# Performance work log

Hardware: AMD Instinct MI355X
Metric: run time of the kernel (lower is better)

The kernel has to match this reference:

```python
import jax, jax.numpy as jnp
import numpy as np
from jax import lax


def _conv(x, w, b):
    # x: [N,C,H,W], w: [O,I,kh,kw], valid conv, stride 1
    y = lax.conv_general_dilated(x, w, (1, 1), 'VALID',
                                 dimension_numbers=('NCHW', 'OIHW', 'NCHW'))
    return y + b[None, :, None, None]


def _maxpool2(x):
    return lax.reduce_window(x, -jnp.inf, lax.max, (1, 1, 2, 2), (1, 1, 2, 2), 'VALID')


def _affine_grid(theta, H, W):
    # torch F.affine_grid, align_corners=False: pixel-center normalized coords
    dt = theta.dtype
    xs = (2.0 * jnp.arange(W, dtype=dt) + 1.0) / W - 1.0  # [W]
    ys = (2.0 * jnp.arange(H, dtype=dt) + 1.0) / H - 1.0  # [H]
    gx = (theta[:, 0, 0][:, None, None] * xs[None, None, :]
          + theta[:, 0, 1][:, None, None] * ys[None, :, None]
          + theta[:, 0, 2][:, None, None])  # [N,H,W]
    gy = (theta[:, 1, 0][:, None, None] * xs[None, None, :]
          + theta[:, 1, 1][:, None, None] * ys[None, :, None]
          + theta[:, 1, 2][:, None, None])  # [N,H,W]
    return gx, gy


def _grid_sample(img, gx, gy):
    # torch F.grid_sample, bilinear, zeros padding, align_corners=False
    N, C, H, W = img.shape
    ix = ((gx + 1.0) * W - 1.0) * 0.5
    iy = ((gy + 1.0) * H - 1.0) * 0.5
    x0 = jnp.floor(ix)
    y0 = jnp.floor(iy)
    x1 = x0 + 1.0
    y1 = y0 + 1.0
    wx1 = ix - x0
    wx0 = 1.0 - wx1
    wy1 = iy - y0
    wy0 = 1.0 - wy1
    flat = img.reshape(N, C, H * W)

    def tap(xf, yf):
        xi = xf.astype(jnp.int32)
        yi = yf.astype(jnp.int32)
        inb = (xi >= 0) & (xi < W) & (yi >= 0) & (yi < H)
        idx = jnp.clip(yi, 0, H - 1) * W + jnp.clip(xi, 0, W - 1)  # [N,H,W]
        v = jnp.take_along_axis(flat, idx.reshape(N, 1, H * W), axis=2)
        return v.reshape(N, C, H, W) * inb.astype(img.dtype)[:, None]

    out = (tap(x0, y0) * (wx0 * wy0)[:, None]
           + tap(x1, y0) * (wx1 * wy0)[:, None]
           + tap(x0, y1) * (wx0 * wy1)[:, None]
           + tap(x1, y1) * (wx1 * wy1)[:, None])
    return out


def setup_inputs() -> dict:
    key = jax.random.key(0)
    ks = jax.random.split(key, 8)
    b, n, d, c = 64, 256, 28, 3
    x = jax.random.normal(ks[0], (b, n, d, d, c), dtype=jnp.float32)
    conv1_w = jax.random.normal(ks[1], (8, 3, 7, 7), dtype=jnp.float32) * 0.08
    conv1_b = jnp.zeros((8,), dtype=jnp.float32)
    conv2_w = jax.random.normal(ks[2], (10, 8, 5, 5), dtype=jnp.float32) * 0.07
    conv2_b = jnp.zeros((10,), dtype=jnp.float32)
    fc1_w = jax.random.normal(ks[3], (32, 90), dtype=jnp.float32) * 0.1
    fc1_b = jnp.zeros((32,), dtype=jnp.float32)
    # fc2 initialized near identity transform (as in the torch module),
    # with a small perturbation so theta depends on the input
    fc2_w = jax.random.normal(ks[4], (6, 32), dtype=jnp.float32) * 0.01
    fc2_b = jnp.array([1.0, 0.0, 0.0, 0.0, 1.0, 0.0], dtype=jnp.float32)
    return {"x": x, "conv1_w": conv1_w, "conv1_b": conv1_b,
            "conv2_w": conv2_w, "conv2_b": conv2_b,
            "fc1_w": fc1_w, "fc1_b": fc1_b,
            "fc2_w": fc2_w, "fc2_b": fc2_b}


def reference(x, conv1_w, conv1_b, conv2_w, conv2_b, fc1_w, fc1_b, fc2_w, fc2_b):
    b, n, d, _, c = x.shape
    xi = x.reshape(-1, d, d, c).transpose(0, 3, 1, 2)  # [b*n, 3, 28, 28]
    # localization net: conv -> maxpool -> relu, twice
    h = jax.nn.relu(_maxpool2(_conv(xi, conv1_w, conv1_b)))   # [N,8,11,11]
    h = jax.nn.relu(_maxpool2(_conv(h, conv2_w, conv2_b)))    # [N,10,3,3]
    h = h.reshape(-1, 10 * 3 * 3)
    h = jax.nn.relu(h @ fc1_w.T + fc1_b)
    theta = (h @ fc2_w.T + fc2_b).reshape(-1, 2, 3)
    gx, gy = _affine_grid(theta, d, d)
    out = _grid_sample(xi, gx, gy)                            # [N,3,28,28]
    return out.transpose(0, 2, 3, 1).reshape(b, n, d, d, c)
```

## Files before the change

### kernel.cpp

```cpp
#include <hip/hip_runtime.h>


typedef _Float16 half2_t __attribute__((ext_vector_type(2)));

static __device__ inline half2_t h2(uint32_t u) {
    union { uint32_t u; half2_t h; } cv; cv.u = u; return cv.h;
}
static __device__ inline uint32_t packh2(float a, float b) {
    union { half2_t h; uint32_t u; } cv;
    cv.h = (half2_t){(_Float16)a, (_Float16)b};
    return cv.u;
}

#if __has_builtin(__builtin_amdgcn_fdot2)
#define FDOT2(a, b, c) __builtin_amdgcn_fdot2((a), (b), (c), false)
#else
#define FDOT2(a, b, c) ((float)(a)[0] * (float)(b)[0] + (float)(a)[1] * (float)(b)[1] + (c))
#endif

#if __has_builtin(__builtin_amdgcn_alignbit)
#define ALIGN16(hi, lo) __builtin_amdgcn_alignbit((hi), (lo), 16)
#else
#define ALIGN16(hi, lo) (((lo) >> 16) | ((hi) << 16))
#endif

__launch_bounds__(256)
__global__ void stn_pack_kernel(
    const float* __restrict__ w2, const float* __restrict__ fc1w,
    uint32_t* __restrict__ w2p, uint32_t* __restrict__ fc1p)
{
    const int t = threadIdx.x;
    for (int k = t; k < 1000; k += 256) {
        const int o = k / 100;
        const int rem = k - 100 * o;
        const int c2kh = rem / 5;
        const int kw = rem - 5 * c2kh;
        const int c2 = c2kh / 5;
        const int kh = c2kh - 5 * c2;
        w2p[k] = packh2(w2[((o * 8 + 2 * c2) * 5 + kh) * 5 + kw],
                        w2[((o * 8 + 2 * c2 + 1) * 5 + kh) * 5 + kw]);
    }
    for (int k = t; k < 1472; k += 256) {
        const int of = k / 46;
        const int p = k - 46 * of;
        uint32_t v = 0;
        if (p < 45) v = packh2(fc1w[of * 90 + 2 * p], fc1w[of * 90 + 2 * p + 1]);
        fc1p[k] = v;
    }
}

__launch_bounds__(256, 4)
__global__ void stn_loc_kernel(
    const float* __restrict__ x,
    const float* __restrict__ w1, const float* __restrict__ b1,
    const uint32_t* __restrict__ w2p, const float* __restrict__ b2,
    const uint32_t* __restrict__ fc1p, const float* __restrict__ fc1b,
    const float* __restrict__ fc2w, const float* __restrict__ fc2b,
    float* __restrict__ theta_ws)
{
    __shared__ __align__(16) _Float16 s_imgh[4][3 * 28 * 40];
    __shared__ __align__(16) uint32_t s_w1p[8 * 21 * 4];
    __shared__ __align__(16) uint32_t s_h1p[4 * 4 * 10 * 12];
    __shared__ __align__(16) uint32_t s_h2p[4][48];
    __shared__ float s_fch[4][32];

    const int t = threadIdx.x;
    const int nb = blockIdx.x;

    for (int im = 0; im < 4; ++im) {
        const float* img = x + ((size_t)(nb * 4 + im)) * 2352;
        for (int p = t; p < 784; p += 256) {
            const int h = p / 28, w = p - 28 * h;
            s_imgh[im][(0 * 28 + h) * 40 + w] = (_Float16)img[3 * p + 0];
            s_imgh[im][(1 * 28 + h) * 40 + w] = (_Float16)img[3 * p + 1];
            s_imgh[im][(2 * 28 + h) * 40 + w] = (_Float16)img[3 * p + 2];
        }
        for (int idx = t; idx < 504; idx += 256) {
            const int cc = idx / 168;
            const int rem = idx - 168 * cc;
            const int hh = rem / 6;
            const int kk = rem - 6 * hh;
            ((uint32_t*)s_imgh[im])[(((cc * 28 + hh) * 40) + 28 + 2 * kk) >> 1] = 0u;
        }
    }
    for (int idx = t; idx < 672; idx += 256) {
        const int o = idx / 84;  const int rem = idx - 84 * o;
        const int c = rem / 28;  const int r2 = rem - 28 * c;
        const int kh = r2 >> 2;  const int p = r2 & 3;
        const int k0 = 2 * p;
        const float* wbase = &w1[((o * 3 + c) * 7 + kh) * 7];
        const float wa = wbase[k0];
        const float wb = (k0 + 1 < 7) ? wbase[k0 + 1] : 0.0f;
        s_w1p[idx] = packh2(wa, wb);
    }
    if (t < 12) s_h2p[t / 3][45 + t % 3] = 0u;
    __syncthreads();

    for (int u = t; u < 704; u += 256) {
        const int im = u / 176;
        const int r  = u - 176 * im;
        const int i = r >> 3, o = r & 7;
        float acc[22];
        #pragma unroll
        for (int j = 0; j < 22; ++j) acc[j] = 0.0f;

        for (int c = 0; c < 3; ++c) {
            #pragma unroll
            for (int kh = 0; kh < 7; ++kh) {
                const uint32_t* rowu =
                    (const uint32_t*)&s_imgh[im][(c * 28 + i + kh) * 40];
                uint32_t E[16];
                {
                    const uint4 a = ((const uint4*)rowu)[0];
                    const uint4 b = ((const uint4*)rowu)[1];
                    const uint4 cq = ((const uint4*)rowu)[2];
                    const uint4 d = ((const uint4*)rowu)[3];
                    E[0] = a.x;  E[1] = a.y;  E[2] = a.z;  E[3] = a.w;
                    E[4] = b.x;  E[5] = b.y;  E[6] = b.z;  E[7] = b.w;
                    E[8] = cq.x; E[9] = cq.y; E[10] = cq.z; E[11] = cq.w;
                    E[12] = d.x; E[13] = d.y; E[14] = d.z; E[15] = d.w;
                }
                uint32_t O[14];
                #pragma unroll
                for (int k = 0; k < 14; ++k)
                    O[k] = ALIGN16(E[k + 1], E[k]);

                const uint4 wq = *(const uint4*)&s_w1p[(o * 21 + c * 7 + kh) * 4];
                const half2_t wp0 = h2(wq.x), wp1 = h2(wq.y);
                const half2_t wp2 = h2(wq.z), wp3 = h2(wq.w);

                #pragma unroll
                for (int j = 0; j < 22; j += 2) {
                    const int b0 = j >> 1;
                    acc[j]     = FDOT2(h2(E[b0]),     wp0, acc[j]);
                    acc[j]     = FDOT2(h2(E[b0 + 1]), wp1, acc[j]);
                    acc[j]     = FDOT2(h2(E[b0 + 2]), wp2, acc[j]);
                    acc[j]     = FDOT2(h2(E[b0 + 3]), wp3, acc[j]);
                    acc[j + 1] = FDOT2(h2(O[b0]),     wp0, acc[j + 1]);
                    acc[j + 1] = FDOT2(h2(O[b0 + 1]), wp1, acc[j + 1]);
                    acc[j + 1] = FDOT2(h2(O[b0 + 2]), wp2, acc[j + 1]);
                    acc[j + 1] = FDOT2(h2(O[b0 + 3]), wp3, acc[j + 1]);
                }
            }
        }
        const float bias = b1[o];
        float hm[11];
        #pragma unroll
        for (int j = 0; j < 11; ++j) hm[j] = fmaxf(acc[2 * j], acc[2 * j + 1]);
        #pragma unroll
        for (int j = 0; j < 11; ++j) {
            float v = __shfl_xor(hm[j], 8);
            hm[j] = fmaxf(hm[j], v);
        }
        if ((i & 1) == 0 && i < 20) {
            const int c2 = o >> 1, u2 = i >> 1;
            _Float16* dst = ((_Float16*)s_h1p)
                          + (((im * 4 + c2) * 10 + u2) * 12) * 2 + (o & 1);
            #pragma unroll
            for (int m = 0; m < 10; ++m)
                dst[2 * m] = (_Float16)fmaxf(hm[m] + bias, 0.0f);
        }
    }
    __syncthreads();

    if (t < 240) {
        const int im = t / 60;
        const int r = t - 60 * im;
        const int o = r / 6, i = r - 6 * (r / 6);
        float acc2[6];
        #pragma unroll
        for (int j = 0; j < 6; ++j) acc2[j] = 0.0f;
        for (int c2 = 0; c2 < 4; ++c2) {
            #pragma unroll
            for (int kh = 0; kh < 5; ++kh) {
                const uint32_t* row = &s_h1p[((im * 4 + c2) * 10 + (i + kh)) * 12];
                uint32_t E[12];
                {
                    const uint4 a = ((const uint4*)row)[0];
                    const uint4 b = ((const uint4*)row)[1];
                    const uint4 cq = ((const uint4*)row)[2];
                    E[0] = a.x;  E[1] = a.y;  E[2] = a.z;  E[3] = a.w;
                    E[4] = b.x;  E[5] = b.y;  E[6] = b.z;  E[7] = b.w;
                    E[8] = cq.x; E[9] = cq.y; E[10] = cq.z; E[11] = cq.w;
                }
                const uint32_t* wb = &w2p[o * 100 + (c2 * 5 + kh) * 5];
                const half2_t w0 = h2(wb[0]), w1_ = h2(wb[1]), w2_ = h2(wb[2]),
                              w3_ = h2(wb[3]), w4_ = h2(wb[4]);
                #pragma unroll
                for (int j = 0; j < 6; ++j) {
                    float a_ = acc2[j];
                    a_ = FDOT2(h2(E[j]),     w0,  a_);
                    a_ = FDOT2(h2(E[j + 1]), w1_, a_);
                    a_ = FDOT2(h2(E[j + 2]), w2_, a_);
                    a_ = FDOT2(h2(E[j + 3]), w3_, a_);
                    a_ = FDOT2(h2(E[j + 4]), w4_, a_);
                    acc2[j] = a_;
                }
            }
        }
        const float bias = b2[o];
        float hp[3];
        #pragma unroll
        for (int q = 0; q < 3; ++q) hp[q] = fmaxf(acc2[2 * q], acc2[2 * q + 1]);
        #pragma unroll
        for (int q = 0; q < 3; ++q) {
            float v = __shfl_xor(hp[q], 1);
            hp[q] = fmaxf(hp[q], v);
        }
        if ((i & 1) == 0) {
            #pragma unroll
            for (int q = 0; q < 3; ++q)
                ((_Float16*)&s_h2p[im][0])[o * 9 + (i >> 1) * 3 + q] =
                    (_Float16)fmaxf(hp[q] + bias, 0.0f);
        }
    }
    __syncthreads();

    {
        const int im = t >> 6;
        const int of = (t >> 1) & 31;
        const int l = t & 1;
        float acc = 0.0f;
        const uint32_t* wr = &fc1p[of * 46];
        #pragma unroll
        for (int m = 0; m < 23; ++m) {
            const int q = l + 2 * m;
            acc = FDOT2(h2(s_h2p[im][q]), h2(wr[q]), acc);
        }
        acc += __shfl_xor(acc, 1);
        if (l == 0) s_fch[im][of] = fmaxf(acc + fc1b[of], 0.0f);
    }
    __syncthreads();

    if (t < 192) {
        const int im = t / 48;
        const int r = t - 48 * im;
        const int of = r >> 3, l = r & 7;
        float acc = 0.0f;
        const float* wr = &fc2w[of * 32];
        #pragma unroll
        for (int m = 0; m < 4; ++m) {
            const int j = l + 8 * m;
            acc += s_fch[im][j] * wr[j];
        }
        acc += __shfl_xor(acc, 1);
        acc += __shfl_xor(acc, 2);
        acc += __shfl_xor(acc, 4);
        if (l == 0) theta_ws[((size_t)(nb * 4 + im)) * 6 + of] = acc + fc2b[of];
    }
}

__launch_bounds__(256)
__global__ void stn_sample_kernel(
    const float* __restrict__ x,
    const float* __restrict__ theta_ws,
    float* __restrict__ out)
{
    const int t = threadIdx.x;
    const int n = blockIdx.x;
    const float* tw = theta_ws + (size_t)n * 6;
    const float t00 = tw[0], t01 = tw[1], t02 = tw[2];
    const float t10 = tw[3], t11 = tw[4], t12 = tw[5];
    const float* img = x + (size_t)n * 2352;
    float* outp = out + (size_t)n * 2352;

    for (int p = t; p < 784; p += 256) {
        int h = p / 28, w = p - 28 * h;
        float xs = (2.0f * w + 1.0f) * (1.0f / 28.0f) - 1.0f;
        float ys = (2.0f * h + 1.0f) * (1.0f / 28.0f) - 1.0f;
        float gx = t00 * xs + t01 * ys + t02;
        float gy = t10 * xs + t11 * ys + t12;
        float ix = ((gx + 1.0f) * 28.0f - 1.0f) * 0.5f;
        float iy = ((gy + 1.0f) * 28.0f - 1.0f) * 0.5f;
        float x0f = floorf(ix), y0f = floorf(iy);
        float wx1 = ix - x0f, wx0 = 1.0f - wx1;
        float wy1 = iy - y0f, wy0 = 1.0f - wy1;
        int x0 = (int)x0f, y0 = (int)y0f;
        int x1 = x0 + 1, y1 = y0 + 1;
        float fx0 = (x0 >= 0 && x0 < 28) ? 1.0f : 0.0f;
        float fx1 = (x1 >= 0 && x1 < 28) ? 1.0f : 0.0f;
        float fy0 = (y0 >= 0 && y0 < 28) ? 1.0f : 0.0f;
        float fy1 = (y1 >= 0 && y1 < 28) ? 1.0f : 0.0f;
        float w00 = wx0 * wy0 * fx0 * fy0;
        float w10 = wx1 * wy0 * fx1 * fy0;
        float w01 = wx0 * wy1 * fx0 * fy1;
        float w11 = wx1 * wy1 * fx1 * fy1;
        int cx0 = min(max(x0, 0), 27), cx1 = min(max(x1, 0), 27);
        int cy0 = min(max(y0, 0), 27), cy1 = min(max(y1, 0), 27);
        const float* p00 = img + (cy0 * 28 + cx0) * 3;
        const float* p10 = img + (cy0 * 28 + cx1) * 3;
        const float* p01 = img + (cy1 * 28 + cx0) * 3;
        const float* p11 = img + (cy1 * 28 + cx1) * 3;
        float* o3 = outp + 3 * p;
        #pragma unroll
        for (int c = 0; c < 3; ++c) {
            o3[c] = p00[c] * w00 + p10[c] * w10 + p01[c] * w01 + p11[c] * w11;
        }
    }
}

extern "C" void kernel_launch(void* const* d_in, const int* in_sizes, int n_in,
                              void* d_out, int out_size, void* d_ws, size_t ws_size,
                              hipStream_t stream) {
    const float* x     = (const float*)d_in[0];
    const float* w1    = (const float*)d_in[1];
    const float* b1    = (const float*)d_in[2];
    const float* w2    = (const float*)d_in[3];
    const float* b2    = (const float*)d_in[4];
    const float* fc1w  = (const float*)d_in[5];
    const float* fc1b  = (const float*)d_in[6];
    const float* fc2w  = (const float*)d_in[7];
    const float* fc2b  = (const float*)d_in[8];
    float* outp  = (float*)d_out;

    float*    theta = (float*)d_ws;
    uint32_t* w2p   = (uint32_t*)d_ws + 98304;
    uint32_t* fc1p  = (uint32_t*)d_ws + 98304 + 1024;

    const int n_img = 64 * 256;
    stn_pack_kernel<<<dim3(1), dim3(256), 0, stream>>>(w2, fc1w, w2p, fc1p);
    stn_loc_kernel<<<dim3(n_img / 4), dim3(256), 0, stream>>>(
        x, w1, b1, w2p, b2, fc1p, fc1b, fc2w, fc2b, theta);
    stn_sample_kernel<<<dim3(n_img), dim3(256), 0, stream>>>(x, theta, outp);
}
```

Baseline: 269.0 us.

## Fuse grid sampling into localization kernel using shared-memory fp16 image

Merges the sampling kernel into the localization kernel: theta is kept in shared memory and bilinear taps read the fp16 image tile already staged in LDS instead of rereading the fp32 input from global memory. This removes a second full pass over the input, the theta workspace round trip and one kernel launch. The sampled values now come from fp16-rounded pixels, which adds precision error to the output. Padding zeroing is also folded into the load loop.

```diff
diff --git a/kernel.cpp b/kernel.cpp
--- a/kernel.cpp
+++ b/kernel.cpp
@@ -50,19 +50,20 @@
 }
 
 __launch_bounds__(256, 4)
-__global__ void stn_loc_kernel(
+__global__ void stn_fused_kernel(
     const float* __restrict__ x,
     const float* __restrict__ w1, const float* __restrict__ b1,
     const uint32_t* __restrict__ w2p, const float* __restrict__ b2,
     const uint32_t* __restrict__ fc1p, const float* __restrict__ fc1b,
     const float* __restrict__ fc2w, const float* __restrict__ fc2b,
-    float* __restrict__ theta_ws)
+    float* __restrict__ out)
 {
     __shared__ __align__(16) _Float16 s_imgh[4][3 * 28 * 40];
     __shared__ __align__(16) uint32_t s_w1p[8 * 21 * 4];
     __shared__ __align__(16) uint32_t s_h1p[4 * 4 * 10 * 12];
     __shared__ __align__(16) uint32_t s_h2p[4][48];
     __shared__ float s_fch[4][32];
+    __shared__ float s_th[4][8];
 
     const int t = threadIdx.x;
     const int nb = blockIdx.x;
@@ -74,13 +75,11 @@
             s_imgh[im][(0 * 28 + h) * 40 + w] = (_Float16)img[3 * p + 0];
             s_imgh[im][(1 * 28 + h) * 40 + w] = (_Float16)img[3 * p + 1];
             s_imgh[im][(2 * 28 + h) * 40 + w] = (_Float16)img[3 * p + 2];
-        }
-        for (int idx = t; idx < 504; idx += 256) {
-            const int cc = idx / 168;
-            const int rem = idx - 168 * cc;
-            const int hh = rem / 6;
-            const int kk = rem - 6 * hh;
-            ((uint32_t*)s_imgh[im])[(((cc * 28 + hh) * 40) + 28 + 2 * kk) >> 1] = 0u;
+            if (w < 12) {
+                s_imgh[im][(0 * 28 + h) * 40 + 28 + w] = (_Float16)0.0f;
+                s_imgh[im][(1 * 28 + h) * 40 + 28 + w] = (_Float16)0.0f;
+                s_imgh[im][(2 * 28 + h) * 40 + 28 + w] = (_Float16)0.0f;
+            }
         }
     }
     for (int idx = t; idx < 672; idx += 256) {
@@ -246,55 +245,47 @@
         acc += __shfl_xor(acc, 1);
         acc += __shfl_xor(acc, 2);
         acc += __shfl_xor(acc, 4);
-        if (l == 0) theta_ws[((size_t)(nb * 4 + im)) * 6 + of] = acc + fc2b[of];
-    }
-}
-
-__launch_bounds__(256)
-__global__ void stn_sample_kernel(
-    const float* __restrict__ x,
-    const float* __restrict__ theta_ws,
-    float* __restrict__ out)
-{
-    const int t = threadIdx.x;
-    const int n = blockIdx.x;
-    const float* tw = theta_ws + (size_t)n * 6;
-    const float t00 = tw[0], t01 = tw[1], t02 = tw[2];
-    const float t10 = tw[3], t11 = tw[4], t12 = tw[5];
-    const float* img = x + (size_t)n * 2352;
-    float* outp = out + (size_t)n * 2352;
-
-    for (int p = t; p < 784; p += 256) {
-        int h = p / 28, w = p - 28 * h;
-        float xs = (2.0f * w + 1.0f) * (1.0f / 28.0f) - 1.0f;
-        float ys = (2.0f * h + 1.0f) * (1.0f / 28.0f) - 1.0f;
-        float gx = t00 * xs + t01 * ys + t02;
-        float gy = t10 * xs + t11 * ys + t12;
-        float ix = ((gx + 1.0f) * 28.0f - 1.0f) * 0.5f;
-        float iy = ((gy + 1.0f) * 28.0f - 1.0f) * 0.5f;
-        float x0f = floorf(ix), y0f = floorf(iy);
-        float wx1 = ix - x0f, wx0 = 1.0f - wx1;
-        float wy1 = iy - y0f, wy0 = 1.0f - wy1;
-        int x0 = (int)x0f, y0 = (int)y0f;
-        int x1 = x0 + 1, y1 = y0 + 1;
-        float fx0 = (x0 >= 0 && x0 < 28) ? 1.0f : 0.0f;
-        float fx1 = (x1 >= 0 && x1 < 28) ? 1.0f : 0.0f;
-        float fy0 = (y0 >= 0 && y0 < 28) ? 1.0f : 0.0f;
-        float fy1 = (y1 >= 0 && y1 < 28) ? 1.0f : 0.0f;
-        float w00 = wx0 * wy0 * fx0 * fy0;
-        float w10 = wx1 * wy0 * fx1 * fy0;
-        float w01 = wx0 * wy1 * fx0 * fy1;
-        float w11 = wx1 * wy1 * fx1 * fy1;
-        int cx0 = min(max(x0, 0), 27), cx1 = min(max(x1, 0), 27);
-        int cy0 = min(max(y0, 0), 27), cy1 = min(max(y1, 0), 27);
-        const float* p00 = img + (cy0 * 28 + cx0) * 3;
-        const float* p10 = img + (cy0 * 28 + cx1) * 3;
-        const float* p01 = img + (cy1 * 28 + cx0) * 3;
-        const float* p11 = img + (cy1 * 28 + cx1) * 3;
-        float* o3 = outp + 3 * p;
+        if (l == 0) s_th[im][of] = acc + fc2b[of];
+    }
+    __syncthreads();
+
+    for (int u = t; u < 3136; u += 256) {
+        const int im = u / 784;
+        const int p = u - 784 * im;
+        const int h = p / 28, w = p - 28 * h;
+        const float t00 = s_th[im][0], t01 = s_th[im][1], t02 = s_th[im][2];
+        const float t10 = s_th[im][3], t11 = s_th[im][4], t12 = s_th[im][5];
+        const float xs = (2.0f * w + 1.0f) * (1.0f / 28.0f) - 1.0f;
+        const float ys = (2.0f * h + 1.0f) * (1.0f / 28.0f) - 1.0f;
+        const float gx = t00 * xs + t01 * ys + t02;
+        const float gy = t10 * xs + t11 * ys + t12;
+        const float ix = ((gx + 1.0f) * 28.0f - 1.0f) * 0.5f;
+        const float iy = ((gy + 1.0f) * 28.0f - 1.0f) * 0.5f;
+        const float x0f = floorf(ix), y0f = floorf(iy);
+        const float wx1 = ix - x0f, wx0 = 1.0f - wx1;
+        const float wy1 = iy - y0f, wy0 = 1.0f - wy1;
+        const int x0 = (int)x0f, y0 = (int)y0f;
+        const int x1 = x0 + 1, y1 = y0 + 1;
+        const float fx0 = (x0 >= 0 && x0 < 28) ? 1.0f : 0.0f;
+        const float fx1 = (x1 >= 0 && x1 < 28) ? 1.0f : 0.0f;
+        const float fy0 = (y0 >= 0 && y0 < 28) ? 1.0f : 0.0f;
+        const float fy1 = (y1 >= 0 && y1 < 28) ? 1.0f : 0.0f;
+        const float w00 = wx0 * wy0 * fx0 * fy0;
+        const float w10 = wx1 * wy0 * fx1 * fy0;
+        const float w01 = wx0 * wy1 * fx0 * fy1;
+        const float w11 = wx1 * wy1 * fx1 * fy1;
+        const int cx0 = min(max(x0, 0), 27), cx1 = min(max(x1, 0), 27);
+        const int cy0 = min(max(y0, 0), 27), cy1 = min(max(y1, 0), 27);
+        const _Float16* imh = s_imgh[im];
+        float* o3 = out + ((size_t)(nb * 4 + im)) * 2352 + 3 * p;
         #pragma unroll
         for (int c = 0; c < 3; ++c) {
-            o3[c] = p00[c] * w00 + p10[c] * w10 + p01[c] * w01 + p11[c] * w11;
+            const _Float16* ic = imh + c * 1120;
+            const float v = (float)ic[cy0 * 40 + cx0] * w00
+                          + (float)ic[cy0 * 40 + cx1] * w10
+                          + (float)ic[cy1 * 40 + cx0] * w01
+                          + (float)ic[cy1 * 40 + cx1] * w11;
+            o3[c] = v;
         }
     }
 }
@@ -311,15 +302,13 @@
     const float* fc1b  = (const float*)d_in[6];
     const float* fc2w  = (const float*)d_in[7];
     const float* fc2b  = (const float*)d_in[8];
-    float* outp  = (float*)d_out;
-
-    float*    theta = (float*)d_ws;
-    uint32_t* w2p   = (uint32_t*)d_ws + 98304;
-    uint32_t* fc1p  = (uint32_t*)d_ws + 98304 + 1024;
+    float* outp = (float*)d_out;
+
+    uint32_t* w2p  = (uint32_t*)d_ws;
+    uint32_t* fc1p = (uint32_t*)d_ws + 1024;
 
     const int n_img = 64 * 256;
     stn_pack_kernel<<<dim3(1), dim3(256), 0, stream>>>(w2, fc1w, w2p, fc1p);
-    stn_loc_kernel<<<dim3(n_img / 4), dim3(256), 0, stream>>>(
-        x, w1, b1, w2p, b2, fc1p, fc1b, fc2w, fc2b, theta);
-    stn_sample_kernel<<<dim3(n_img), dim3(256), 0, stream>>>(x, theta, outp);
-}
+    stn_fused_kernel<<<dim3(n_img / 4), dim3(256), 0, stream>>>(
+        x, w1, b1, w2p, b2, fc1p, fc1b, fc2w, fc2b, outp);
+}
```

Result: faster. 263.3 us (-2.1%).
